# Optimization experiments

Hardware: AMD Instinct MI355X
Metric: run time of the kernel (lower is better)

## Reference

```python
import jax, jax.numpy as jnp
import numpy as np

# UMAP a,b fitted offline for spread=5, min_dist=0.001 (curve_fit of 1/(1+a x^(2b)))
ALPHA = 0.1520
BETA = 0.7900
N_NODES = 50000
IN_DIM = 128
HID = 64
OUT_DIM = 2
N_EDGES = 800000


def setup_inputs() -> dict:
    key = jax.random.key(0)
    ks = jax.random.split(key, 8)
    feats = jax.random.normal(ks[0], (N_NODES, IN_DIM), dtype=jnp.float32)
    W1 = jax.random.normal(ks[1], (IN_DIM, HID), dtype=jnp.float32) / np.sqrt(IN_DIM)
    b1 = jnp.zeros((HID,), dtype=jnp.float32)
    W2 = jax.random.normal(ks[2], (HID, OUT_DIM), dtype=jnp.float32) / np.sqrt(HID)
    b2 = jnp.zeros((OUT_DIM,), dtype=jnp.float32)
    edge_index = jax.random.randint(ks[3], (2, N_EDGES), 0, N_NODES, dtype=jnp.int64)
    row_neg = jax.random.randint(ks[4], (N_EDGES,), 0, N_NODES, dtype=jnp.int64)
    col_neg = jax.random.randint(ks[5], (N_EDGES,), 0, N_NODES, dtype=jnp.int64)
    return {"features": feats, "W1": W1, "b1": b1, "W2": W2, "b2": b2,
            "edge_index": edge_index, "row_neg": row_neg, "col_neg": col_neg}


def _gcn_norm(edge_index, n_nodes):
    # add self-loops, symmetric normalization D^-1/2 (A+I) D^-1/2
    loops = jnp.arange(n_nodes, dtype=edge_index.dtype)
    row = jnp.concatenate([edge_index[0], loops])
    col = jnp.concatenate([edge_index[1], loops])
    deg = jax.ops.segment_sum(jnp.ones_like(row, dtype=jnp.float32), row,
                              num_segments=n_nodes)
    dinv = jnp.where(deg > 0, jax.lax.rsqrt(deg), 0.0)
    norm = dinv[row] * dinv[col]  # [E + N]
    return row, col, norm


def _gcn_conv(x, W, b, row, col, norm, n_nodes):
    h = x @ W                      # [N, out]
    msg = h[col] * norm[:, None]   # edge-indexed gather (irregular access)
    agg = jax.ops.segment_sum(msg, row, num_segments=n_nodes)
    return agg + b


def _forward(features, W1, b1, W2, b2, edge_index, row_neg, col_neg):
    n = features.shape[0]
    row, col, norm = _gcn_norm(edge_index, n)
    h = jax.nn.relu(_gcn_conv(features, W1, b1, row, col, norm, n))
    emb = _gcn_conv(h, W2, b2, row, col, norm, n)  # [N, 2]
    # pairwise L2 distances at positive edges and negative samples
    pos_diff = emb[edge_index[0]] - emb[edge_index[1]]
    neg_diff = emb[row_neg] - emb[col_neg]
    eps = 1e-12  # guards grad at zero distance (torch.norm subgradient is 0 there)
    pos_d = jnp.sqrt(jnp.sum(pos_diff * pos_diff, axis=1) + eps)
    neg_d = jnp.sqrt(jnp.sum(neg_diff * neg_diff, axis=1) + eps)
    lowdim_dist = jnp.concatenate([pos_d, neg_d], axis=0)  # [2E]
    q = 1.0 / (1.0 + ALPHA * jnp.power(lowdim_dist, 2.0 * BETA))
    return emb, q


def reference(features, W1, b1, W2, b2, edge_index, row_neg, col_neg):
    return _forward(features, W1, b1, W2, b2, edge_index, row_neg, col_neg)
```

## Files before the change

kernel.cpp:

```cpp
#include <hip/hip_runtime.h>
#include <hip/hip_fp16.h>
#include <math.h>

constexpr int   NN     = 50000;
constexpr int   IN_DIM = 128;
constexpr int   HID    = 64;
constexpr int   NE     = 800000;
constexpr float ALPHA  = 0.1520f;
constexpr float BETA   = 0.7900f;

constexpr int RSH = 7;
constexpr int RPB = 1 << RSH;
constexpr int NB  = (NN + RPB - 1) / RPB;
constexpr int NBP = 512;
constexpr int CH  = 4096;
constexpr int NCH = (NE + CH - 1) / CH;
constexpr int CAP = 4096;

__global__ __launch_bounds__(256) void k_bhist(const int* __restrict__ row,
                                               int* __restrict__ bpart) {
    __shared__ int h[NBP];
    int t = threadIdx.x;
    for (int i = t; i < NBP; i += 256) h[i] = 0;
    __syncthreads();
    int e0 = blockIdx.x * CH;
#pragma unroll
    for (int i = 0; i < 16; ++i) {
        int e = e0 + i * 256 + t;
        if (e < NE) atomicAdd(&h[row[e] >> RSH], 1);
    }
    __syncthreads();
    for (int b = t; b < NB; b += 256) bpart[b * NCH + blockIdx.x] = h[b];
}

__global__ void k_bsum(const int* __restrict__ bpart, int* __restrict__ bhist) {
    int b = blockIdx.x;
    int v = 0;
    for (int i = threadIdx.x; i < NCH; i += 64) v += bpart[b * NCH + i];
#pragma unroll
    for (int d = 32; d >= 1; d >>= 1) v += __shfl_xor(v, d);
    if (threadIdx.x == 0) bhist[b] = v;
}

__global__ void k_bscan(const int* __restrict__ bhist, int* __restrict__ boffs,
                        int* __restrict__ bcur) {
    __shared__ int s[NBP];
    int t = threadIdx.x;
    s[t]       = (t < NB) ? bhist[t] : 0;
    s[t + 256] = (t + 256 < NB) ? bhist[t + 256] : 0;
    __syncthreads();
    for (int d = 1; d < NBP; d <<= 1) {
        int v0 = (t >= d) ? s[t - d] : 0;
        int v1 = (t + 256 >= d) ? s[t + 256 - d] : 0;
        __syncthreads();
        s[t] += v0;
        s[t + 256] += v1;
        __syncthreads();
    }
    if (t < NB)       { int e = s[t] - bhist[t];             boffs[t] = e;       bcur[t] = e; }
    if (t + 256 < NB) { int e = s[t + 256] - bhist[t + 256]; boffs[t + 256] = e; bcur[t + 256] = e; }
    if (t == 0) boffs[NB] = NE;
}

__global__ __launch_bounds__(256) void k_binfill(const int* __restrict__ row,
                                                 const int* __restrict__ col,
                                                 int* __restrict__ bcur,
                                                 unsigned int* __restrict__ bedge) {
    __shared__ int hist[NBP];
    __shared__ int scn[NBP];
    __shared__ int ebase[NB];
    __shared__ int gbase[NB];
    __shared__ int lcur[NB];
    __shared__ unsigned int pk[CH];
    __shared__ int gof[CH];

    int t = threadIdx.x;
    int e0 = blockIdx.x * CH;
    int rw[16], cl[16];
#pragma unroll
    for (int i = 0; i < 16; ++i) {
        int e = e0 + i * 256 + t;
        if (e < NE) { rw[i] = row[e]; cl[i] = col[e]; } else rw[i] = -1;
    }
    for (int i = t; i < NBP; i += 256) hist[i] = 0;
    __syncthreads();
#pragma unroll
    for (int i = 0; i < 16; ++i)
        if (rw[i] >= 0) atomicAdd(&hist[rw[i] >> RSH], 1);
    __syncthreads();
    scn[t] = hist[t];
    scn[t + 256] = hist[t + 256];
    __syncthreads();
    for (int d = 1; d < NBP; d <<= 1) {
        int v0 = (t >= d) ? scn[t - d] : 0;
        int v1 = (t + 256 >= d) ? scn[t + 256 - d] : 0;
        __syncthreads();
        scn[t] += v0;
        scn[t + 256] += v1;
        __syncthreads();
    }
    for (int b = t; b < NB; b += 256) {
        int h  = hist[b];
        int eb = scn[b] - h;
        ebase[b] = eb;
        lcur[b]  = eb;
        gbase[b] = h ? atomicAdd(&bcur[b], h) : 0;
    }
    __syncthreads();
#pragma unroll
    for (int i = 0; i < 16; ++i) {
        if (rw[i] >= 0) {
            int b = rw[i] >> RSH;
            int s = atomicAdd(&lcur[b], 1);
            pk[s]  = ((unsigned int)(rw[i] & (RPB - 1)) << 17) | (unsigned int)cl[i];
            gof[s] = gbase[b] + (s - ebase[b]);
        }
    }
    __syncthreads();
    int nval = min(CH, NE - e0);
    for (int s = t; s < nval; s += 256) bedge[gof[s]] = pk[s];
}

__global__ __launch_bounds__(256) void k_bucket(const unsigned int* __restrict__ bedge,
                                                const int* __restrict__ boffs,
                                                int* __restrict__ offs,
                                                float* __restrict__ dinv,
                                                int* __restrict__ scol) {
    __shared__ int cnt[RPB];
    __shared__ int loff[RPB];
    __shared__ int wtot[2];
    __shared__ unsigned int ld[CAP];
    __shared__ int buf[CAP];

    int b = blockIdx.x, t = threadIdx.x;
    int beg = boffs[b], end = boffs[b + 1];
    int m = end - beg;
    int nbase = b << RSH;

    if (t < RPB) cnt[t] = 0;
    __syncthreads();

    if (m <= CAP) {
        for (int i = t; i < m; i += 256) {
            unsigned int mm = bedge[beg + i];
            ld[i] = mm;
            atomicAdd(&cnt[mm >> 17], 1);
        }
        __syncthreads();
        if (t < RPB) {
            int v = cnt[t];
            int x = v;
#pragma unroll
            for (int d = 1; d < 64; d <<= 1) {
                int y = __shfl_up(x, d);
                if ((t & 63) >= d) x += y;
            }
            if ((t & 63) == 63) wtot[t >> 6] = x;
            loff[t] = x - v;
        }
        __syncthreads();
        if (t >= 64 && t < RPB) loff[t] += wtot[0];
        __syncthreads();
        if (t < RPB) {
            int n = nbase + t;
            if (n < NN) {
                offs[n] = beg + loff[t];
                dinv[n] = rsqrtf((float)(cnt[t] + 1));
            }
        }
        if (b == NB - 1 && t == 0) offs[NN] = NE;
        if (t < RPB) cnt[t] = loff[t];
        __syncthreads();
        for (int i = t; i < m; i += 256) {
            unsigned int mm = ld[i];
            int s = atomicAdd(&cnt[mm >> 17], 1);
            buf[s] = (int)(mm & 0x1FFFFu);
        }
        __syncthreads();
        for (int i = t; i < m; i += 256) scol[beg + i] = buf[i];
    } else {
        for (int i = t; i < m; i += 256)
            atomicAdd(&cnt[bedge[beg + i] >> 17], 1);
        __syncthreads();
        if (t < RPB) {
            int v = cnt[t];
            int x = v;
#pragma unroll
            for (int d = 1; d < 64; d <<= 1) {
                int y = __shfl_up(x, d);
                if ((t & 63) >= d) x += y;
            }
            if ((t & 63) == 63) wtot[t >> 6] = x;
            loff[t] = x - v;
        }
        __syncthreads();
        if (t >= 64 && t < RPB) loff[t] += wtot[0];
        __syncthreads();
        if (t < RPB) {
            int n = nbase + t;
            if (n < NN) {
                offs[n] = beg + loff[t];
                dinv[n] = rsqrtf((float)(cnt[t] + 1));
            }
        }
        if (b == NB - 1 && t == 0) offs[NN] = NE;
        if (t < RPB) cnt[t] = loff[t];
        __syncthreads();
        for (int i = t; i < m; i += 256) {
            unsigned int mm = bedge[beg + i];
            int s = atomicAdd(&cnt[mm >> 17], 1);
            scol[beg + s] = (int)(mm & 0x1FFFFu);
        }
    }
}

__global__ __launch_bounds__(256) void k_gemm1(const float* __restrict__ feat,
                                               const float* __restrict__ W1,
                                               const float* __restrict__ dinv,
                                               __half* __restrict__ h1s) {
    __shared__ float sW[IN_DIM * HID];
    __shared__ float sF[16][IN_DIM];
    int t = threadIdx.x;

    const float4* W4  = (const float4*)W1;
    float4*       sW4 = (float4*)sW;
#pragma unroll
    for (int i = 0; i < 8; ++i) sW4[t + i * 256] = W4[t + i * 256];

    int n0 = blockIdx.x * 16;
    const float4* F4  = (const float4*)(feat + (size_t)n0 * IN_DIM);
    float4*       sF4 = (float4*)&sF[0][0];
    sF4[t]       = F4[t];
    sF4[t + 256] = F4[t + 256];
    __syncthreads();

    int c = t & 63;
    int g = t >> 6;
    float acc[4] = {0.f, 0.f, 0.f, 0.f};
    for (int k = 0; k < IN_DIM; ++k) {
        float w = sW[k * HID + c];
#pragma unroll
        for (int i = 0; i < 4; ++i) acc[i] += sF[g * 4 + i][k] * w;
    }
#pragma unroll
    for (int i = 0; i < 4; ++i) {
        int n = n0 + g * 4 + i;
        h1s[(size_t)n * HID + c] = __float2half(acc[i] * dinv[n]);
    }
}

__global__ __launch_bounds__(256) void k_agg1(const int* __restrict__ offs,
                                              const int* __restrict__ scol,
                                              const float* __restrict__ dinv,
                                              const __half* __restrict__ h1s,
                                              const float* __restrict__ b1,
                                              const float* __restrict__ W2,
                                              float* __restrict__ h2s) {
    int n    = blockIdx.x * 4 + (threadIdx.x >> 6);
    int lane = threadIdx.x & 63;
    if (n >= NN) return;
    int g  = lane >> 4;
    int cq = lane & 15;
    int beg = offs[n], end = offs[n + 1];

    const uint2* H = (const uint2*)h1s;
    float a0 = 0.f, a1 = 0.f, a2 = 0.f, a3 = 0.f;
    int k = beg + g;
    for (; k + 4 < end; k += 8) {
        uint2 va = H[(size_t)scol[k] * 16 + cq];
        uint2 vb = H[(size_t)scol[k + 4] * 16 + cq];
        float2 fa0 = __half22float2(*(__half2*)&va.x);
        float2 fa1 = __half22float2(*(__half2*)&va.y);
        float2 fb0 = __half22float2(*(__half2*)&vb.x);
        float2 fb1 = __half22float2(*(__half2*)&vb.y);
        a0 += fa0.x + fb0.x;
        a1 += fa0.y + fb0.y;
        a2 += fa1.x + fb1.x;
        a3 += fa1.y + fb1.y;
    }
    if (k < end) {
        uint2 va = H[(size_t)scol[k] * 16 + cq];
        float2 fa0 = __half22float2(*(__half2*)&va.x);
        float2 fa1 = __half22float2(*(__half2*)&va.y);
        a0 += fa0.x; a1 += fa0.y; a2 += fa1.x; a3 += fa1.y;
    }
    a0 += __shfl_xor(a0, 16); a0 += __shfl_xor(a0, 32);
    a1 += __shfl_xor(a1, 16); a1 += __shfl_xor(a1, 32);
    a2 += __shfl_xor(a2, 16); a2 += __shfl_xor(a2, 32);
    a3 += __shfl_xor(a3, 16); a3 += __shfl_xor(a3, 32);

    uint2 sv = H[(size_t)n * 16 + cq];
    float2 s0 = __half22float2(*(__half2*)&sv.x);
    float2 s1 = __half22float2(*(__half2*)&sv.y);
    float di = dinv[n];
    float4 b14 = ((const float4*)b1)[cq];
    a0 = fmaxf(di * (a0 + s0.x) + b14.x, 0.f);
    a1 = fmaxf(di * (a1 + s0.y) + b14.y, 0.f);
    a2 = fmaxf(di * (a2 + s1.x) + b14.z, 0.f);
    a3 = fmaxf(di * (a3 + s1.y) + b14.w, 0.f);

    float4 w01 = ((const float4*)W2)[cq * 2];
    float4 w23 = ((const float4*)W2)[cq * 2 + 1];
    float p0 = a0 * w01.x + a1 * w01.z + a2 * w23.x + a3 * w23.z;
    float p1 = a0 * w01.y + a1 * w01.w + a2 * w23.y + a3 * w23.w;
#pragma unroll
    for (int d = 8; d >= 1; d >>= 1) {
        p0 += __shfl_xor(p0, d);
        p1 += __shfl_xor(p1, d);
    }
    if (lane == 0) {
        h2s[(size_t)n * 2 + 0] = di * p0;
        h2s[(size_t)n * 2 + 1] = di * p1;
    }
}

__global__ __launch_bounds__(256) void k_agg2(const int* __restrict__ offs,
                                              const int* __restrict__ scol,
                                              const float* __restrict__ dinv,
                                              const float* __restrict__ h2s,
                                              const float* __restrict__ b2,
                                              float* __restrict__ emb) {
    int wid  = threadIdx.x >> 6;
    int lane = threadIdx.x & 63;
    int n = blockIdx.x * 16 + wid * 4 + (lane >> 4);
    int e = lane & 15;
    const float2* h22 = (const float2*)h2s;
    float e0 = 0.f, e1 = 0.f;
    int beg = 0, end = 0;
    if (n < NN) { beg = offs[n]; end = offs[n + 1]; }
    for (int k = beg + e; k < end; k += 16) {
        float2 v = h22[scol[k]];
        e0 += v.x;
        e1 += v.y;
    }
#pragma unroll
    for (int d = 8; d >= 1; d >>= 1) {
        e0 += __shfl_xor(e0, d);
        e1 += __shfl_xor(e1, d);
    }
    if (e == 0 && n < NN) {
        float di = dinv[n];
        float2 self = h22[n];
        emb[(size_t)n * 2 + 0] = di * (e0 + self.x) + b2[0];
        emb[(size_t)n * 2 + 1] = di * (e1 + self.y) + b2[1];
    }
}

__global__ void k_q(const int* __restrict__ pr, const int* __restrict__ pc,
                    const int* __restrict__ nr, const int* __restrict__ nc,
                    const float* __restrict__ emb, float* __restrict__ q) {
    int e = blockIdx.x * blockDim.x + threadIdx.x;
    if (e >= 2 * NE) return;
    int a, b;
    if (e < NE) { a = pr[e]; b = pc[e]; }
    else        { a = nr[e - NE]; b = nc[e - NE]; }
    const float2* e2 = (const float2*)emb;
    float2 A = e2[a], B = e2[b];
    float dx = A.x - B.x, dy = A.y - B.y;
    float d = sqrtf(dx * dx + dy * dy + 1e-12f);
    float p = exp2f(2.0f * BETA * log2f(d));
    q[e] = 1.0f / (1.0f + ALPHA * p);
}

extern "C" void kernel_launch(void* const* d_in, const int* in_sizes, int n_in,
                              void* d_out, int out_size, void* d_ws, size_t ws_size,
                              hipStream_t stream) {
    const float* feat = (const float*)d_in[0];
    const float* W1   = (const float*)d_in[1];
    const float* b1   = (const float*)d_in[2];
    const float* W2   = (const float*)d_in[3];
    const float* b2   = (const float*)d_in[4];
    const int*   ei   = (const int*)d_in[5];
    const int*   nrw  = (const int*)d_in[6];
    const int*   ncl  = (const int*)d_in[7];
    const int* row = ei;
    const int* col = ei + NE;

    char* cur = (char*)d_ws;
    auto alloc = [&](size_t bytes) -> char* {
        char* p = cur;
        cur += (bytes + 255) & ~(size_t)255;
        return p;
    };
    int*          bpart = (int*)alloc(sizeof(int) * (size_t)NB * NCH);
    int*          bhist = (int*)alloc(sizeof(int) * NB);
    int*          boffs = (int*)alloc(sizeof(int) * (NB + 1));
    int*          bcur  = (int*)alloc(sizeof(int) * NB);
    int*          offs  = (int*)alloc(sizeof(int) * (NN + 1));
    float*        dinv  = (float*)alloc(sizeof(float) * NN);
    unsigned int* bedge = (unsigned int*)alloc(sizeof(unsigned int) * NE);
    int*          scol  = (int*)alloc(sizeof(int) * NE);
    float*        h2s   = (float*)alloc(sizeof(float) * (size_t)NN * 2);
    __half*       h1s   = (__half*)alloc(sizeof(__half) * (size_t)NN * HID);

    float* emb = (float*)d_out;
    float* q   = (float*)d_out + (size_t)NN * 2;

    k_bhist  <<<NCH, 256, 0, stream>>>(row, bpart);
    k_bsum   <<<NB, 64, 0, stream>>>(bpart, bhist);
    k_bscan  <<<1, 256, 0, stream>>>(bhist, boffs, bcur);
    k_binfill<<<NCH, 256, 0, stream>>>(row, col, bcur, bedge);
    k_bucket <<<NB, 256, 0, stream>>>(bedge, boffs, offs, dinv, scol);

    k_gemm1<<<NN / 16, 256, 0, stream>>>(feat, W1, dinv, h1s);

    k_agg1<<<(NN + 3) / 4, 256, 0, stream>>>(offs, scol, dinv, h1s, b1, W2, h2s);
    k_agg2<<<(NN + 15) / 16, 256, 0, stream>>>(offs, scol, dinv, h2s, b2, emb);

    k_q<<<(2 * NE + 255) / 256, 256, 0, stream>>>(row, col, nrw, ncl, emb, q);
}
```

Before: 107.8 us.

## Replace atomic bin cursors with per-chunk exclusive prefix offsets and vectorize loads

Drops the separate bin-sum kernel and folds the per-chunk histogram reduction into the single-block scan, which writes exclusive per-(bin,chunk) prefix offsets in place. The fill kernel now reads deterministic global offsets instead of doing atomicAdd on bin cursors, and both the histogram and fill kernels load row/col with int4 vector reads over contiguous 16-edge runs per thread. The layer-1 aggregation loop is unrolled to four gathers per iteration for more memory-level parallelism. The risk is that the single-block scan now serially walks about 196 chunks per bin per thread, which may cost more than the launch it removes.

```diff
diff --git a/kernel.cpp b/kernel.cpp
--- a/kernel.cpp
+++ b/kernel.cpp
@@ -23,31 +23,42 @@
     int t = threadIdx.x;
     for (int i = t; i < NBP; i += 256) h[i] = 0;
     __syncthreads();
-    int e0 = blockIdx.x * CH;
-#pragma unroll
-    for (int i = 0; i < 16; ++i) {
-        int e = e0 + i * 256 + t;
-        if (e < NE) atomicAdd(&h[row[e] >> RSH], 1);
+    int base = blockIdx.x * CH + t * 16;
+    if (base + 15 < NE) {
+        const int4* R = (const int4*)(row + base);
+#pragma unroll
+        for (int i = 0; i < 4; ++i) {
+            int4 r = R[i];
+            atomicAdd(&h[r.x >> RSH], 1);
+            atomicAdd(&h[r.y >> RSH], 1);
+            atomicAdd(&h[r.z >> RSH], 1);
+            atomicAdd(&h[r.w >> RSH], 1);
+        }
+    } else {
+        for (int i = 0; i < 16; ++i) {
+            int e = base + i;
+            if (e < NE) atomicAdd(&h[row[e] >> RSH], 1);
+        }
     }
     __syncthreads();
     for (int b = t; b < NB; b += 256) bpart[b * NCH + blockIdx.x] = h[b];
 }
 
-__global__ void k_bsum(const int* __restrict__ bpart, int* __restrict__ bhist) {
-    int b = blockIdx.x;
-    int v = 0;
-    for (int i = threadIdx.x; i < NCH; i += 64) v += bpart[b * NCH + i];
-#pragma unroll
-    for (int d = 32; d >= 1; d >>= 1) v += __shfl_xor(v, d);
-    if (threadIdx.x == 0) bhist[b] = v;
-}
-
-__global__ void k_bscan(const int* __restrict__ bhist, int* __restrict__ boffs,
-                        int* __restrict__ bcur) {
+__global__ __launch_bounds__(256) void k_bscan(int* __restrict__ bpart,
+                                               int* __restrict__ boffs) {
     __shared__ int s[NBP];
     int t = threadIdx.x;
-    s[t]       = (t < NB) ? bhist[t] : 0;
-    s[t + 256] = (t + 256 < NB) ? bhist[t + 256] : 0;
+    int tot0 = 0, tot1 = 0;
+    {
+        int* p = bpart + (size_t)t * NCH;
+        for (int c = 0; c < NCH; ++c) { int v = p[c]; p[c] = tot0; tot0 += v; }
+    }
+    if (t + 256 < NB) {
+        int* p = bpart + (size_t)(t + 256) * NCH;
+        for (int c = 0; c < NCH; ++c) { int v = p[c]; p[c] = tot1; tot1 += v; }
+    }
+    s[t]       = tot0;
+    s[t + 256] = (t + 256 < NB) ? tot1 : 0;
     __syncthreads();
     for (int d = 1; d < NBP; d <<= 1) {
         int v0 = (t >= d) ? s[t - d] : 0;
@@ -57,14 +68,15 @@
         s[t + 256] += v1;
         __syncthreads();
     }
-    if (t < NB)       { int e = s[t] - bhist[t];             boffs[t] = e;       bcur[t] = e; }
-    if (t + 256 < NB) { int e = s[t + 256] - bhist[t + 256]; boffs[t + 256] = e; bcur[t + 256] = e; }
+    if (t < NB)       boffs[t]       = s[t] - tot0;
+    if (t + 256 < NB) boffs[t + 256] = s[t + 256] - tot1;
     if (t == 0) boffs[NB] = NE;
 }
 
 __global__ __launch_bounds__(256) void k_binfill(const int* __restrict__ row,
                                                  const int* __restrict__ col,
-                                                 int* __restrict__ bcur,
+                                                 const int* __restrict__ bpart,
+                                                 const int* __restrict__ boffs,
                                                  unsigned int* __restrict__ bedge) {
     __shared__ int hist[NBP];
     __shared__ int scn[NBP];
@@ -75,12 +87,23 @@
     __shared__ int gof[CH];
 
     int t = threadIdx.x;
-    int e0 = blockIdx.x * CH;
+    int base = blockIdx.x * CH + t * 16;
     int rw[16], cl[16];
-#pragma unroll
-    for (int i = 0; i < 16; ++i) {
-        int e = e0 + i * 256 + t;
-        if (e < NE) { rw[i] = row[e]; cl[i] = col[e]; } else rw[i] = -1;
+    if (base + 15 < NE) {
+        const int4* R = (const int4*)(row + base);
+        const int4* C = (const int4*)(col + base);
+#pragma unroll
+        for (int i = 0; i < 4; ++i) {
+            int4 r = R[i];
+            int4 c = C[i];
+            rw[4 * i + 0] = r.x; rw[4 * i + 1] = r.y; rw[4 * i + 2] = r.z; rw[4 * i + 3] = r.w;
+            cl[4 * i + 0] = c.x; cl[4 * i + 1] = c.y; cl[4 * i + 2] = c.z; cl[4 * i + 3] = c.w;
+        }
+    } else {
+        for (int i = 0; i < 16; ++i) {
+            int e = base + i;
+            if (e < NE) { rw[i] = row[e]; cl[i] = col[e]; } else rw[i] = -1;
+        }
     }
     for (int i = t; i < NBP; i += 256) hist[i] = 0;
     __syncthreads();
@@ -104,7 +127,7 @@
         int eb = scn[b] - h;
         ebase[b] = eb;
         lcur[b]  = eb;
-        gbase[b] = h ? atomicAdd(&bcur[b], h) : 0;
+        gbase[b] = boffs[b] + bpart[b * NCH + blockIdx.x];
     }
     __syncthreads();
 #pragma unroll
@@ -117,7 +140,7 @@
         }
     }
     __syncthreads();
-    int nval = min(CH, NE - e0);
+    int nval = min(CH, NE - blockIdx.x * CH);
     for (int s = t; s < nval; s += 256) bedge[gof[s]] = pk[s];
 }
 
@@ -266,23 +289,26 @@
     const uint2* H = (const uint2*)h1s;
     float a0 = 0.f, a1 = 0.f, a2 = 0.f, a3 = 0.f;
     int k = beg + g;
-    for (; k + 4 < end; k += 8) {
-        uint2 va = H[(size_t)scol[k] * 16 + cq];
-        uint2 vb = H[(size_t)scol[k + 4] * 16 + cq];
-        float2 fa0 = __half22float2(*(__half2*)&va.x);
-        float2 fa1 = __half22float2(*(__half2*)&va.y);
-        float2 fb0 = __half22float2(*(__half2*)&vb.x);
-        float2 fb1 = __half22float2(*(__half2*)&vb.y);
-        a0 += fa0.x + fb0.x;
-        a1 += fa0.y + fb0.y;
-        a2 += fa1.x + fb1.x;
-        a3 += fa1.y + fb1.y;
-    }
-    if (k < end) {
-        uint2 va = H[(size_t)scol[k] * 16 + cq];
-        float2 fa0 = __half22float2(*(__half2*)&va.x);
-        float2 fa1 = __half22float2(*(__half2*)&va.y);
-        a0 += fa0.x; a1 += fa0.y; a2 += fa1.x; a3 += fa1.y;
+    for (; k + 12 < end; k += 16) {
+        int c0 = scol[k], c1 = scol[k + 4], c2 = scol[k + 8], c3 = scol[k + 12];
+        uint2 v0 = H[(size_t)c0 * 16 + cq];
+        uint2 v1 = H[(size_t)c1 * 16 + cq];
+        uint2 v2 = H[(size_t)c2 * 16 + cq];
+        uint2 v3 = H[(size_t)c3 * 16 + cq];
+        float2 f0a = __half22float2(*(__half2*)&v0.x), f0b = __half22float2(*(__half2*)&v0.y);
+        float2 f1a = __half22float2(*(__half2*)&v1.x), f1b = __half22float2(*(__half2*)&v1.y);
+        float2 f2a = __half22float2(*(__half2*)&v2.x), f2b = __half22float2(*(__half2*)&v2.y);
+        float2 f3a = __half22float2(*(__half2*)&v3.x), f3b = __half22float2(*(__half2*)&v3.y);
+        a0 += (f0a.x + f1a.x) + (f2a.x + f3a.x);
+        a1 += (f0a.y + f1a.y) + (f2a.y + f3a.y);
+        a2 += (f0b.x + f1b.x) + (f2b.x + f3b.x);
+        a3 += (f0b.y + f1b.y) + (f2b.y + f3b.y);
+    }
+    for (; k < end; k += 4) {
+        uint2 v = H[(size_t)scol[k] * 16 + cq];
+        float2 fa = __half22float2(*(__half2*)&v.x);
+        float2 fb = __half22float2(*(__half2*)&v.y);
+        a0 += fa.x; a1 += fa.y; a2 += fb.x; a3 += fb.y;
     }
     a0 += __shfl_xor(a0, 16); a0 += __shfl_xor(a0, 32);
     a1 += __shfl_xor(a1, 16); a1 += __shfl_xor(a1, 32);
@@ -383,9 +409,7 @@
         return p;
     };
     int*          bpart = (int*)alloc(sizeof(int) * (size_t)NB * NCH);
-    int*          bhist = (int*)alloc(sizeof(int) * NB);
     int*          boffs = (int*)alloc(sizeof(int) * (NB + 1));
-    int*          bcur  = (int*)alloc(sizeof(int) * NB);
     int*          offs  = (int*)alloc(sizeof(int) * (NN + 1));
     float*        dinv  = (float*)alloc(sizeof(float) * NN);
     unsigned int* bedge = (unsigned int*)alloc(sizeof(unsigned int) * NE);
@@ -397,9 +421,8 @@
     float* q   = (float*)d_out + (size_t)NN * 2;
 
     k_bhist  <<<NCH, 256, 0, stream>>>(row, bpart);
-    k_bsum   <<<NB, 64, 0, stream>>>(bpart, bhist);
-    k_bscan  <<<1, 256, 0, stream>>>(bhist, boffs, bcur);
-    k_binfill<<<NCH, 256, 0, stream>>>(row, col, bcur, bedge);
+    k_bscan  <<<1, 256, 0, stream>>>(bpart, boffs);
+    k_binfill<<<NCH, 256, 0, stream>>>(row, col, bpart, boffs, bedge);
     k_bucket <<<NB, 256, 0, stream>>>(bedge, boffs, offs, dinv, scol);
 
     k_gemm1<<<NN / 16, 256, 0, stream>>>(feat, W1, dinv, h1s);
```

After: 132.4 us. +22.8%, slower.
